# Optimization experiments

Hardware: AMD Instinct MI355X
Metric: run time of the kernel (lower is better)

## Reference

```python
import jax, jax.numpy as jnp
import numpy as np

B, T_ENC, IN, H, SEQ_OUT = 1024, 50, 99, 2112, 25


def _lstm_cell(x, h, c, W_ih, b_ih, W_hh, b_hh):
    # gates: [B, 4H], torch LSTMCell gate order is i, f, g, o
    gates = x @ W_ih.T + b_ih + h @ W_hh.T + b_hh
    i, f, g, o = jnp.split(gates, 4, axis=-1)
    c_new = jax.nn.sigmoid(f) * c + jax.nn.sigmoid(i) * jnp.tanh(g)
    h_new = jax.nn.sigmoid(o) * jnp.tanh(c_new)
    return h_new, c_new


def setup_inputs() -> dict:
    key = jax.random.key(0)
    ks = jax.random.split(key, 14)
    s = 0.04
    return {
        "hidden_states": jax.random.normal(ks[0], (B, T_ENC, H), jnp.float32),
        "cell_states": jax.random.normal(ks[1], (B, T_ENC, H), jnp.float32),
        "global_t_state": jax.random.normal(ks[2], (B, H), jnp.float32),
        "p": jax.random.normal(ks[3], (B, 1, IN), jnp.float32),
        "W_ih0": jax.random.normal(ks[4], (4 * H, IN), jnp.float32) * s,
        "b_ih0": jax.random.normal(ks[5], (4 * H,), jnp.float32) * s,
        "W_hh0": jax.random.normal(ks[6], (4 * H, H), jnp.float32) * s,
        "b_hh0": jax.random.normal(ks[7], (4 * H,), jnp.float32) * s,
        "W_ih1": jax.random.normal(ks[8], (4 * H, H), jnp.float32) * s,
        "b_ih1": jax.random.normal(ks[9], (4 * H,), jnp.float32) * s,
        "W_hh1": jax.random.normal(ks[10], (4 * H, H), jnp.float32) * s,
        "b_hh1": jax.random.normal(ks[11], (4 * H,), jnp.float32) * s,
        "W_out": jax.random.normal(ks[12], (H, IN), jnp.float32) * s,
        "b_out": jax.random.normal(ks[13], (IN,), jnp.float32) * s,
    }


def reference(hidden_states, cell_states, global_t_state, p,
              W_ih0, b_ih0, W_hh0, b_hh0,
              W_ih1, b_ih1, W_hh1, b_hh1,
              W_out, b_out):
    # initial states: layer 0 uses mean over encoder hidden states,
    # layer 1 uses mean over [global_t_state ; hidden_states]
    h0 = hidden_states.mean(axis=1)                                   # [B, H]
    h1 = jnp.concatenate((global_t_state[:, None, :], hidden_states), axis=1).mean(axis=1)
    c0 = cell_states.mean(axis=1)
    c1 = c0
    pre0 = p[:, 0, :]                                                 # seed input [B, IN]

    def step(carry, _):
        h0, c0, h1, c1, prev = carry
        h0n, c0n = _lstm_cell(prev, h0, c0, W_ih0, b_ih0, W_hh0, b_hh0)
        h1n, c1n = _lstm_cell(h0n, h1, c1, W_ih1, b_ih1, W_hh1, b_hh1)
        pre = h1n @ W_out + b_out + prev                              # residual on cell-0 input
        return (h0n, c0n, h1n, c1n, pre), pre

    _, pres = jax.lax.scan(step, (h0, c0, h1, c1, pre0), None, length=SEQ_OUT)
    return pres.transpose(1, 0, 2)                                    # [B, SEQ_OUT, IN]
```

## Files before the change

### kernel.cpp

```cpp
#include <hip/hip_runtime.h>

#define B_    1024
#define H_    2112
#define FH    8448
#define IN_   99
#define TENC  50
#define SEQ   25
#define K0    2240
#define K1    4224
#define LDX0  2240
#define LDX1  4224

typedef __bf16 bf16;
typedef __bf16 bf16x8 __attribute__((ext_vector_type(8)));
typedef __bf16 bf16x4 __attribute__((ext_vector_type(4)));
typedef float  f32x4  __attribute__((ext_vector_type(4)));

__device__ __forceinline__ void gload_lds16(const void* g, void* l) {
  __builtin_amdgcn_global_load_lds(
      (const __attribute__((address_space(1))) void*)g,
      (__attribute__((address_space(3))) void*)l, 16, 0, 0);
}

__device__ __forceinline__ float sigf(float x) { return 1.f / (1.f + __expf(-x)); }
__device__ __forceinline__ float tanhfast(float x) { return 1.f - 2.f / (__expf(2.f * x) + 1.f); }

__global__ __launch_bounds__(128, 3)
void lstm_gemm_cell(const bf16* __restrict__ X, int lda, int K,
                    const bf16* __restrict__ W,
                    const float* __restrict__ bsum,
                    float* __restrict__ Cst,
                    bf16* __restrict__ d1, int ld1,
                    bf16* __restrict__ d2, int ld2)
{
  __shared__ __align__(16) bf16 As[128 * 64];
  __shared__ __align__(16) bf16 Bs[64 * 64];

  const int mb  = blockIdx.x & 7;
  const int hb  = blockIdx.x >> 3;
  const int hc0 = hb * 16;
  const int m0  = mb * 128;

  const int tid  = threadIdx.x;
  const int srow = tid >> 3;
  const int scol = ((tid & 7) ^ (srow & 7)) * 8;

  const bf16* Ab = X + (size_t)(m0 + srow) * lda + scol;
  const bf16* Bb = W + (size_t)(hc0 + srow) * K + scol;

  const int lane = tid & 63;
  const int w    = tid >> 6;
  const int lr   = lane & 15, lq = lane >> 4;
  const int xs   = lr & 7;
  const int cof0 = (lq ^ xs) * 8;
  const int cof1 = ((4 + lq) ^ xs) * 8;

  f32x4 acc[4][4];
#pragma unroll
  for (int a = 0; a < 4; ++a)
#pragma unroll
    for (int b = 0; b < 4; ++b) acc[a][b] = (f32x4){0.f, 0.f, 0.f, 0.f};

  const int KT = K >> 6;
  for (int kt = 0; kt < KT; ++kt) {
    const int ko = kt * 64;
#pragma unroll
    for (int it = 0; it < 8; ++it)
      gload_lds16(Ab + (size_t)it * 16 * lda + ko, &As[it * 1024 + tid * 8]);
#pragma unroll
    for (int it = 0; it < 4; ++it)
      gload_lds16(Bb + (size_t)it * H_ * K + ko, &Bs[it * 1024 + tid * 8]);
    __syncthreads();

    bf16x8 af[4][2], bfr[4][2];
#pragma unroll
    for (int mi = 0; mi < 4; ++mi) {
      const int r = (w * 64 + mi * 16 + lr) * 64;
      af[mi][0] = *(const bf16x8*)&As[r + cof0];
      af[mi][1] = *(const bf16x8*)&As[r + cof1];
    }
#pragma unroll
    for (int nf = 0; nf < 4; ++nf) {
      const int r = (nf * 16 + lr) * 64;
      bfr[nf][0] = *(const bf16x8*)&Bs[r + cof0];
      bfr[nf][1] = *(const bf16x8*)&Bs[r + cof1];
    }
#pragma unroll
    for (int mi = 0; mi < 4; ++mi)
#pragma unroll
      for (int nf = 0; nf < 4; ++nf)
#pragma unroll
        for (int kc = 0; kc < 2; ++kc)
          acc[mi][nf] = __builtin_amdgcn_mfma_f32_16x16x32_bf16(
              af[mi][kc], bfr[nf][kc], acc[mi][nf], 0, 0, 0);
    __syncthreads();
  }

  const int hc = hc0 + lr;
  const float bi  = bsum[hc];
  const float bff = bsum[H_ + hc];
  const float bg  = bsum[2 * H_ + hc];
  const float bo  = bsum[3 * H_ + hc];

#pragma unroll
  for (int mi = 0; mi < 4; ++mi) {
#pragma unroll
    for (int r = 0; r < 4; ++r) {
      const int m = m0 + w * 64 + mi * 16 + lq * 4 + r;
      const float gi = acc[mi][0][r] + bi;
      const float gf = acc[mi][1][r] + bff;
      const float gg = acc[mi][2][r] + bg;
      const float go = acc[mi][3][r] + bo;
      const size_t ci = (size_t)m * H_ + hc;
      const float c_old = Cst[ci];
      const float cn = sigf(gf) * c_old + sigf(gi) * tanhfast(gg);
      const float hn = sigf(go) * tanhfast(cn);
      Cst[ci] = cn;
      const bf16 hb2 = (bf16)hn;
      d1[(size_t)m * ld1 + hc] = hb2;
      if (d2) d2[(size_t)m * ld2 + hc] = hb2;
    }
  }
}

__global__ __launch_bounds__(256, 1)
void out_gemm(const bf16* __restrict__ Hin,
              const bf16* __restrict__ Wo,
              const float* __restrict__ b_out,
              float* __restrict__ prev,
              bf16* __restrict__ X0n,
              float* __restrict__ out, int t)
{
  __shared__ float red[4][4][112];
  const int tid = threadIdx.x;
  const int m0 = blockIdx.x * 4;
  const int lane = tid & 63, wv = tid >> 6;
  const int lr = lane & 15, lq = lane >> 4, lk = lq * 8;

  f32x4 acc[7];
#pragma unroll
  for (int b = 0; b < 7; ++b) acc[b] = (f32x4){0.f, 0.f, 0.f, 0.f};

  const int start = (wv == 0) ? 0 : (1 + wv * 8);
  const int cnt = (wv == 0) ? 9 : 8;

  for (int kt = start; kt < start + cnt; ++kt) {
    const int ko = kt * 64;
    bf16x8 av[2], bv[7][2];
#pragma unroll
    for (int kc = 0; kc < 2; ++kc)
      av[kc] = *(const bf16x8*)&Hin[(size_t)(m0 + (lr & 3)) * LDX1 + ko + kc * 32 + lk];
#pragma unroll
    for (int nf = 0; nf < 7; ++nf)
#pragma unroll
      for (int kc = 0; kc < 2; ++kc)
        bv[nf][kc] = *(const bf16x8*)&Wo[(size_t)(nf * 16 + lr) * H_ + ko + kc * 32 + lk];
#pragma unroll
    for (int nf = 0; nf < 7; ++nf)
#pragma unroll
      for (int kc = 0; kc < 2; ++kc)
        acc[nf] = __builtin_amdgcn_mfma_f32_16x16x32_bf16(av[kc], bv[nf][kc], acc[nf], 0, 0, 0);
  }

  if (lq == 0) {
#pragma unroll
    for (int nf = 0; nf < 7; ++nf)
#pragma unroll
      for (int r = 0; r < 4; ++r)
        red[wv][r][nf * 16 + lr] = acc[nf][r];
  }
  __syncthreads();

  for (int idx = tid; idx < 4 * 112; idx += 256) {
    const int ml = idx / 112, n = idx - ml * 112;
    if (n < IN_) {
      const int m = m0 + ml;
      float s = red[0][ml][n] + red[1][ml][n] + red[2][ml][n] + red[3][ml][n] + b_out[n];
      const float pre = s + prev[m * 112 + n];
      prev[m * 112 + n] = pre;
      out[((size_t)m * SEQ + t) * IN_ + n] = pre;
      X0n[(size_t)m * LDX0 + n] = (bf16)pre;
    }
  }
}

__global__ void init_state(const float* __restrict__ hs, const float* __restrict__ cs,
                           const float* __restrict__ gts,
                           bf16* __restrict__ X0a, bf16* __restrict__ X1a,
                           float* __restrict__ c0, float* __restrict__ c1)
{
  const int h4 = blockIdx.x * 256 + threadIdx.x;
  if (h4 >= 528) return;
  const int b = blockIdx.y;
  const float4* hp = (const float4*)(hs + (size_t)b * TENC * H_) + h4;
  const float4* cp = (const float4*)(cs + (size_t)b * TENC * H_) + h4;
  float4 sh = {0.f, 0.f, 0.f, 0.f}, sc = {0.f, 0.f, 0.f, 0.f};
  for (int tt = 0; tt < TENC; ++tt) {
    float4 a = hp[tt * 528];
    sh.x += a.x; sh.y += a.y; sh.z += a.z; sh.w += a.w;
    float4 c = cp[tt * 528];
    sc.x += c.x; sc.y += c.y; sc.z += c.z; sc.w += c.w;
  }
  const float4 g = ((const float4*)(gts + (size_t)b * H_))[h4];
  const float4 c0v = {sc.x / 50.f, sc.y / 50.f, sc.z / 50.f, sc.w / 50.f};
  ((float4*)(c0 + (size_t)b * H_))[h4] = c0v;
  ((float4*)(c1 + (size_t)b * H_))[h4] = c0v;
  bf16x4 h0b = {(bf16)(sh.x / 50.f), (bf16)(sh.y / 50.f), (bf16)(sh.z / 50.f), (bf16)(sh.w / 50.f)};
  *(bf16x4*)&X0a[(size_t)b * LDX0 + 128 + h4 * 4] = h0b;
  bf16x4 h1b = {(bf16)((sh.x + g.x) / 51.f), (bf16)((sh.y + g.y) / 51.f),
                (bf16)((sh.z + g.z) / 51.f), (bf16)((sh.w + g.w) / 51.f)};
  *(bf16x4*)&X1a[(size_t)b * LDX1 + 2112 + h4 * 4] = h1b;
}

__global__ void init_prev(const float* __restrict__ p, float* __restrict__ prev,
                          bf16* __restrict__ X0a, bf16* __restrict__ X0b)
{
  const int idx = blockIdx.x * 256 + threadIdx.x;
  const int b = idx >> 7, n = idx & 127;
  const float v = (n < IN_) ? p[(size_t)b * IN_ + n] : 0.f;
  if (n < 112) prev[b * 112 + n] = v;
  X0a[(size_t)b * LDX0 + n] = (bf16)v;
  X0b[(size_t)b * LDX0 + n] = (bf16)0.f;
}

__global__ void pack_w0(const float* __restrict__ Wih, const float* __restrict__ Whh,
                        bf16* __restrict__ Wc)
{
  const int n = blockIdx.x;
  const float* a = Wih + (size_t)n * IN_;
  const float* b = Whh + (size_t)n * H_;
  bf16* d = Wc + (size_t)n * K0;
  for (int k = threadIdx.x; k < K0; k += 256) {
    float v = (k < IN_) ? a[k] : ((k >= 128) ? b[k - 128] : 0.f);
    d[k] = (bf16)v;
  }
}

__global__ void pack_w1(const float* __restrict__ Wih, const float* __restrict__ Whh,
                        bf16* __restrict__ Wc)
{
  const int n = blockIdx.x;
  bf16* d = Wc + (size_t)n * K1;
  for (int k = threadIdx.x; k < K1; k += 256)
    d[k] = (bf16)((k < H_) ? Wih[(size_t)n * H_ + k] : Whh[(size_t)n * H_ + k - H_]);
}

__global__ void pack_wo(const float* __restrict__ W, bf16* __restrict__ Wo)
{
  const int n = blockIdx.x;
  for (int k = threadIdx.x; k < H_; k += 256)
    Wo[(size_t)n * H_ + k] = (n < IN_) ? (bf16)W[(size_t)k * IN_ + n] : (bf16)0.f;
}

__global__ void pack_bias(const float* __restrict__ bi0, const float* __restrict__ bh0,
                          const float* __restrict__ bi1, const float* __restrict__ bh1,
                          float* __restrict__ bs0, float* __restrict__ bs1)
{
  const int i = blockIdx.x * 256 + threadIdx.x;
  if (i < FH) { bs0[i] = bi0[i] + bh0[i]; bs1[i] = bi1[i] + bh1[i]; }
}

extern "C" void kernel_launch(void* const* d_in, const int* in_sizes, int n_in,
                              void* d_out, int out_size, void* d_ws, size_t ws_size,
                              hipStream_t stream)
{
  (void)in_sizes; (void)n_in; (void)out_size; (void)ws_size;
  const float* hs   = (const float*)d_in[0];
  const float* cs   = (const float*)d_in[1];
  const float* gts  = (const float*)d_in[2];
  const float* p    = (const float*)d_in[3];
  const float* Wih0 = (const float*)d_in[4];
  const float* bih0 = (const float*)d_in[5];
  const float* Whh0 = (const float*)d_in[6];
  const float* bhh0 = (const float*)d_in[7];
  const float* Wih1 = (const float*)d_in[8];
  const float* bih1 = (const float*)d_in[9];
  const float* Whh1 = (const float*)d_in[10];
  const float* bhh1 = (const float*)d_in[11];
  const float* Wout = (const float*)d_in[12];
  const float* bout = (const float*)d_in[13];
  float* out = (float*)d_out;

  char* ws = (char*)d_ws;
  size_t off = 0;
  auto alloc = [&](size_t bytes) -> void* {
    void* q = ws + off; off += (bytes + 255) & ~(size_t)255; return q;
  };
  bf16* Wc0 = (bf16*)alloc((size_t)FH * K0 * 2);
  bf16* Wc1 = (bf16*)alloc((size_t)FH * K1 * 2);
  bf16* Wo  = (bf16*)alloc((size_t)112 * H_ * 2);
  float* bs0 = (float*)alloc((size_t)FH * 4);
  float* bs1 = (float*)alloc((size_t)FH * 4);
  bf16* X0[2] = {(bf16*)alloc((size_t)B_ * LDX0 * 2), (bf16*)alloc((size_t)B_ * LDX0 * 2)};
  bf16* X1[2] = {(bf16*)alloc((size_t)B_ * LDX1 * 2), (bf16*)alloc((size_t)B_ * LDX1 * 2)};
  float* c0  = (float*)alloc((size_t)B_ * H_ * 4);
  float* c1  = (float*)alloc((size_t)B_ * H_ * 4);
  float* prev = (float*)alloc((size_t)B_ * 112 * 4);

  pack_w0<<<FH, 256, 0, stream>>>(Wih0, Whh0, Wc0);
  pack_w1<<<FH, 256, 0, stream>>>(Wih1, Whh1, Wc1);
  pack_wo<<<112, 256, 0, stream>>>(Wout, Wo);
  pack_bias<<<(FH + 255) / 256, 256, 0, stream>>>(bih0, bhh0, bih1, bhh1, bs0, bs1);
  init_prev<<<(B_ * 128) / 256, 256, 0, stream>>>(p, prev, X0[0], X0[1]);
  init_state<<<dim3(3, B_), 256, 0, stream>>>(hs, cs, gts, X0[0], X1[0], c0, c1);

  for (int t = 0; t < SEQ; ++t) {
    const int cur = t & 1, nxt = cur ^ 1;
    lstm_gemm_cell<<<1056, 128, 0, stream>>>(
        X0[cur], LDX0, K0, Wc0, bs0, c0, X1[cur], LDX1, X0[nxt] + 128, LDX0);
    lstm_gemm_cell<<<1056, 128, 0, stream>>>(
        X1[cur], LDX1, K1, Wc1, bs1, c1, X1[nxt] + 2112, LDX1, (bf16*)nullptr, 0);
    out_gemm<<<256, 256, 0, stream>>>(X1[nxt] + 2112, Wo, bout, prev, X0[nxt], out, t);
  }
}
```

Baseline: 5.315 ms.

## Pre-pack LSTM weights in MFMA fragment order and load directly to registers

Weights are repacked once into per-tile MFMA fragment order so each lane loads its B fragments straight from global memory into registers, dropping the Bs LDS buffer and its staging loads. Block indices are also remapped so consecutive blocks share the same weight tile across the 8 M-blocks rather than the same A rows, aiming for better L2 reuse of weights. The trade-off is that global-to-register weight loads now sit on each k-step's critical path with no LDS double-buffering, and the per-k-step LDS footprint shrinks.

```diff
diff --git a/kernel.cpp b/kernel.cpp
--- a/kernel.cpp
+++ b/kernel.cpp
@@ -10,6 +10,9 @@
 #define K1    4224
 #define LDX0  2240
 #define LDX1  4224
+#define KT0   35
+#define KT1   66
+#define HB_   132
 
 typedef __bf16 bf16;
 typedef __bf16 bf16x8 __attribute__((ext_vector_type(8)));
@@ -27,26 +30,24 @@
 
 __global__ __launch_bounds__(128, 3)
 void lstm_gemm_cell(const bf16* __restrict__ X, int lda, int K,
-                    const bf16* __restrict__ W,
+                    const bf16* __restrict__ Wpk,
                     const float* __restrict__ bsum,
                     float* __restrict__ Cst,
                     bf16* __restrict__ d1, int ld1,
                     bf16* __restrict__ d2, int ld2)
 {
   __shared__ __align__(16) bf16 As[128 * 64];
-  __shared__ __align__(16) bf16 Bs[64 * 64];
-
-  const int mb  = blockIdx.x & 7;
-  const int hb  = blockIdx.x >> 3;
+
+  const int vid = (blockIdx.x & 7) * 132 + (blockIdx.x >> 3);
+  const int hb  = vid >> 3;
   const int hc0 = hb * 16;
-  const int m0  = mb * 128;
+  const int m0  = (vid & 7) * 128;
 
   const int tid  = threadIdx.x;
   const int srow = tid >> 3;
   const int scol = ((tid & 7) ^ (srow & 7)) * 8;
 
   const bf16* Ab = X + (size_t)(m0 + srow) * lda + scol;
-  const bf16* Bb = W + (size_t)(hc0 + srow) * K + scol;
 
   const int lane = tid & 63;
   const int w    = tid >> 6;
@@ -55,35 +56,36 @@
   const int cof0 = (lq ^ xs) * 8;
   const int cof1 = ((4 + lq) ^ xs) * 8;
 
+  const int KT = K >> 6;
+  const bf16* Wp = Wpk + (size_t)hb * KT * 4096 + lane * 8;
+
   f32x4 acc[4][4];
 #pragma unroll
   for (int a = 0; a < 4; ++a)
 #pragma unroll
     for (int b = 0; b < 4; ++b) acc[a][b] = (f32x4){0.f, 0.f, 0.f, 0.f};
 
-  const int KT = K >> 6;
   for (int kt = 0; kt < KT; ++kt) {
     const int ko = kt * 64;
 #pragma unroll
     for (int it = 0; it < 8; ++it)
       gload_lds16(Ab + (size_t)it * 16 * lda + ko, &As[it * 1024 + tid * 8]);
-#pragma unroll
-    for (int it = 0; it < 4; ++it)
-      gload_lds16(Bb + (size_t)it * H_ * K + ko, &Bs[it * 1024 + tid * 8]);
+
+    const bf16* Wt = Wp + (size_t)kt * 4096;
+    bf16x8 bfr[4][2];
+#pragma unroll
+    for (int nf = 0; nf < 4; ++nf) {
+      bfr[nf][0] = *(const bf16x8*)&Wt[(nf * 2 + 0) * 512];
+      bfr[nf][1] = *(const bf16x8*)&Wt[(nf * 2 + 1) * 512];
+    }
     __syncthreads();
 
-    bf16x8 af[4][2], bfr[4][2];
+    bf16x8 af[4][2];
 #pragma unroll
     for (int mi = 0; mi < 4; ++mi) {
       const int r = (w * 64 + mi * 16 + lr) * 64;
       af[mi][0] = *(const bf16x8*)&As[r + cof0];
       af[mi][1] = *(const bf16x8*)&As[r + cof1];
-    }
-#pragma unroll
-    for (int nf = 0; nf < 4; ++nf) {
-      const int r = (nf * 16 + lr) * 64;
-      bfr[nf][0] = *(const bf16x8*)&Bs[r + cof0];
-      bfr[nf][1] = *(const bf16x8*)&Bs[r + cof1];
     }
 #pragma unroll
     for (int mi = 0; mi < 4; ++mi)
@@ -223,26 +225,54 @@
   X0b[(size_t)b * LDX0 + n] = (bf16)0.f;
 }
 
-__global__ void pack_w0(const float* __restrict__ Wih, const float* __restrict__ Whh,
-                        bf16* __restrict__ Wc)
-{
-  const int n = blockIdx.x;
-  const float* a = Wih + (size_t)n * IN_;
-  const float* b = Whh + (size_t)n * H_;
-  bf16* d = Wc + (size_t)n * K0;
-  for (int k = threadIdx.x; k < K0; k += 256) {
-    float v = (k < IN_) ? a[k] : ((k >= 128) ? b[k - 128] : 0.f);
-    d[k] = (bf16)v;
-  }
-}
-
-__global__ void pack_w1(const float* __restrict__ Wih, const float* __restrict__ Whh,
-                        bf16* __restrict__ Wc)
-{
-  const int n = blockIdx.x;
-  bf16* d = Wc + (size_t)n * K1;
-  for (int k = threadIdx.x; k < K1; k += 256)
-    d[k] = (bf16)((k < H_) ? Wih[(size_t)n * H_ + k] : Whh[(size_t)n * H_ + k - H_]);
+__global__ void pack_w0_frag(const float* __restrict__ Wih, const float* __restrict__ Whh,
+                             bf16* __restrict__ Wpk)
+{
+  const int kt = blockIdx.x, hb = blockIdx.y;
+  const int lane = threadIdx.x;
+  const int lr = lane & 15, lq = lane >> 4;
+  bf16* dst = Wpk + (((size_t)hb * KT0 + kt) * 8) * 512 + lane * 8;
+#pragma unroll
+  for (int fi = 0; fi < 8; ++fi) {
+    const int nf = fi >> 1, kc = fi & 1;
+    const int row = nf * H_ + hb * 16 + lr;
+    const int k0 = kt * 64 + kc * 32 + lq * 8;
+    bf16x8 v;
+#pragma unroll
+    for (int e = 0; e < 8; ++e) {
+      const int k = k0 + e;
+      float f;
+      if (k < IN_)        f = Wih[(size_t)row * IN_ + k];
+      else if (k < 128)   f = 0.f;
+      else                f = Whh[(size_t)row * H_ + (k - 128)];
+      v[e] = (bf16)f;
+    }
+    *(bf16x8*)(dst + fi * 512) = v;
+  }
+}
+
+__global__ void pack_w1_frag(const float* __restrict__ Wih, const float* __restrict__ Whh,
+                             bf16* __restrict__ Wpk)
+{
+  const int kt = blockIdx.x, hb = blockIdx.y;
+  const int lane = threadIdx.x;
+  const int lr = lane & 15, lq = lane >> 4;
+  bf16* dst = Wpk + (((size_t)hb * KT1 + kt) * 8) * 512 + lane * 8;
+#pragma unroll
+  for (int fi = 0; fi < 8; ++fi) {
+    const int nf = fi >> 1, kc = fi & 1;
+    const int row = nf * H_ + hb * 16 + lr;
+    const int k0 = kt * 64 + kc * 32 + lq * 8;
+    bf16x8 v;
+#pragma unroll
+    for (int e = 0; e < 8; ++e) {
+      const int k = k0 + e;
+      const float f = (k < H_) ? Wih[(size_t)row * H_ + k]
+                               : Whh[(size_t)row * H_ + (k - H_)];
+      v[e] = (bf16)f;
+    }
+    *(bf16x8*)(dst + fi * 512) = v;
+  }
 }
 
 __global__ void pack_wo(const float* __restrict__ W, bf16* __restrict__ Wo)
@@ -286,8 +316,8 @@
   auto alloc = [&](size_t bytes) -> void* {
     void* q = ws + off; off += (bytes + 255) & ~(size_t)255; return q;
   };
-  bf16* Wc0 = (bf16*)alloc((size_t)FH * K0 * 2);
-  bf16* Wc1 = (bf16*)alloc((size_t)FH * K1 * 2);
+  bf16* Wc0 = (bf16*)alloc((size_t)HB_ * KT0 * 4096 * 2);
+  bf16* Wc1 = (bf16*)alloc((size_t)HB_ * KT1 * 4096 * 2);
   bf16* Wo  = (bf16*)alloc((size_t)112 * H_ * 2);
   float* bs0 = (float*)alloc((size_t)FH * 4);
   float* bs1 = (float*)alloc((size_t)FH * 4);
@@ -297,8 +327,8 @@
   float* c1  = (float*)alloc((size_t)B_ * H_ * 4);
   float* prev = (float*)alloc((size_t)B_ * 112 * 4);
 
-  pack_w0<<<FH, 256, 0, stream>>>(Wih0, Whh0, Wc0);
-  pack_w1<<<FH, 256, 0, stream>>>(Wih1, Whh1, Wc1);
+  pack_w0_frag<<<dim3(KT0, HB_), 64, 0, stream>>>(Wih0, Whh0, Wc0);
+  pack_w1_frag<<<dim3(KT1, HB_), 64, 0, stream>>>(Wih1, Whh1, Wc1);
   pack_wo<<<112, 256, 0, stream>>>(Wout, Wo);
   pack_bias<<<(FH + 255) / 256, 256, 0, stream>>>(bih0, bhh0, bih1, bhh1, bs0, bs1);
   init_prev<<<(B_ * 128) / 256, 256, 0, stream>>>(p, prev, X0[0], X0[1]);
```

After: 5.012 ms. 1.06x faster.

## Double-buffer LSTM gate GEMM with larger tiles and remapped block order

Applied to the files above, without the earlier changes.

Rewrites the fused LSTM gate GEMM to use 256-thread blocks computing 128x128 tiles (32 hidden units × 4 gates) with K-step 32 and double-buffered LDS, so the next tile's async loads overlap the current MFMAs. It also remaps the block index so consecutive blocks share weight slices across the batch tiles. The XOR swizzle is dropped, which may introduce LDS bank conflicts, and fewer, larger blocks reduce the number of waves available to hide latency.

```diff
diff --git a/kernel.cpp b/kernel.cpp
--- a/kernel.cpp
+++ b/kernel.cpp
@@ -25,7 +25,7 @@
 __device__ __forceinline__ float sigf(float x) { return 1.f / (1.f + __expf(-x)); }
 __device__ __forceinline__ float tanhfast(float x) { return 1.f - 2.f / (__expf(2.f * x) + 1.f); }
 
-__global__ __launch_bounds__(128, 3)
+__global__ __launch_bounds__(256, 2)
 void lstm_gemm_cell(const bf16* __restrict__ X, int lda, int K,
                     const bf16* __restrict__ W,
                     const float* __restrict__ bsum,
@@ -33,27 +33,28 @@
                     bf16* __restrict__ d1, int ld1,
                     bf16* __restrict__ d2, int ld2)
 {
-  __shared__ __align__(16) bf16 As[128 * 64];
-  __shared__ __align__(16) bf16 Bs[64 * 64];
-
-  const int mb  = blockIdx.x & 7;
-  const int hb  = blockIdx.x >> 3;
-  const int hc0 = hb * 16;
-  const int m0  = mb * 128;
+  __shared__ __align__(16) bf16 As0[128 * 32];
+  __shared__ __align__(16) bf16 As1[128 * 32];
+  __shared__ __align__(16) bf16 Bs0[128 * 32];
+  __shared__ __align__(16) bf16 Bs1[128 * 32];
+
+  const int vid = (blockIdx.x & 7) * 66 + (blockIdx.x >> 3);
+  const int hb  = vid >> 3;
+  const int hc0 = hb * 32;
+  const int m0  = (vid & 7) * 128;
 
   const int tid  = threadIdx.x;
-  const int srow = tid >> 3;
-  const int scol = ((tid & 7) ^ (srow & 7)) * 8;
+  const int srow = tid >> 2;
+  const int scol = (tid & 3) * 8;
 
   const bf16* Ab = X + (size_t)(m0 + srow) * lda + scol;
-  const bf16* Bb = W + (size_t)(hc0 + srow) * K + scol;
+  const bf16* Bb = W + ((size_t)((srow >> 5) * H_ + hc0 + (srow & 31))) * K + scol;
+  const size_t HK2 = (size_t)2 * H_ * K;
 
   const int lane = tid & 63;
-  const int w    = tid >> 6;
-  const int lr   = lane & 15, lq = lane >> 4;
-  const int xs   = lr & 7;
-  const int cof0 = (lq ^ xs) * 8;
-  const int cof1 = ((4 + lq) ^ xs) * 8;
+  const int wv = tid >> 6;
+  const int wm = wv >> 1, wn = wv & 1;
+  const int lr = lane & 15, lq = lane >> 4;
 
   f32x4 acc[4][4];
 #pragma unroll
@@ -61,42 +62,45 @@
 #pragma unroll
     for (int b = 0; b < 4; ++b) acc[a][b] = (f32x4){0.f, 0.f, 0.f, 0.f};
 
-  const int KT = K >> 6;
-  for (int kt = 0; kt < KT; ++kt) {
-    const int ko = kt * 64;
-#pragma unroll
-    for (int it = 0; it < 8; ++it)
-      gload_lds16(Ab + (size_t)it * 16 * lda + ko, &As[it * 1024 + tid * 8]);
-#pragma unroll
-    for (int it = 0; it < 4; ++it)
-      gload_lds16(Bb + (size_t)it * H_ * K + ko, &Bs[it * 1024 + tid * 8]);
+#define STAGE(kt, AD, BD) do {                                              \
+    const int ko_ = (kt) * 32;                                              \
+    gload_lds16(Ab + (size_t)0 * lda + ko_,  &AD[0 * 2048 + tid * 8]);      \
+    gload_lds16(Ab + (size_t)64 * lda + ko_, &AD[1 * 2048 + tid * 8]);      \
+    gload_lds16(Bb + ko_,                    &BD[0 * 2048 + tid * 8]);      \
+    gload_lds16(Bb + HK2 + ko_,              &BD[1 * 2048 + tid * 8]);      \
+  } while (0)
+
+#define COMPUTE(AS, BS) do {                                                \
+    bf16x8 af_[4], bf_[4];                                                  \
+    _Pragma("unroll")                                                       \
+    for (int mi = 0; mi < 4; ++mi)                                          \
+      af_[mi] = *(const bf16x8*)&AS[(wm * 64 + mi * 16 + lr) * 32 + lq * 8];\
+    _Pragma("unroll")                                                       \
+    for (int nf = 0; nf < 4; ++nf)                                          \
+      bf_[nf] = *(const bf16x8*)&BS[(nf * 32 + wn * 16 + lr) * 32 + lq * 8];\
+    _Pragma("unroll")                                                       \
+    for (int mi = 0; mi < 4; ++mi)                                          \
+      _Pragma("unroll")                                                     \
+      for (int nf = 0; nf < 4; ++nf)                                        \
+        acc[mi][nf] = __builtin_amdgcn_mfma_f32_16x16x32_bf16(              \
+            af_[mi], bf_[nf], acc[mi][nf], 0, 0, 0);                        \
+  } while (0)
+
+  const int KT = K >> 5;
+  STAGE(0, As0, Bs0);
+  __syncthreads();
+  for (int kt = 0; kt < KT; kt += 2) {
+    STAGE(kt + 1, As1, Bs1);
+    COMPUTE(As0, Bs0);
     __syncthreads();
-
-    bf16x8 af[4][2], bfr[4][2];
-#pragma unroll
-    for (int mi = 0; mi < 4; ++mi) {
-      const int r = (w * 64 + mi * 16 + lr) * 64;
-      af[mi][0] = *(const bf16x8*)&As[r + cof0];
-      af[mi][1] = *(const bf16x8*)&As[r + cof1];
-    }
-#pragma unroll
-    for (int nf = 0; nf < 4; ++nf) {
-      const int r = (nf * 16 + lr) * 64;
-      bfr[nf][0] = *(const bf16x8*)&Bs[r + cof0];
-      bfr[nf][1] = *(const bf16x8*)&Bs[r + cof1];
-    }
-#pragma unroll
-    for (int mi = 0; mi < 4; ++mi)
-#pragma unroll
-      for (int nf = 0; nf < 4; ++nf)
-#pragma unroll
-        for (int kc = 0; kc < 2; ++kc)
-          acc[mi][nf] = __builtin_amdgcn_mfma_f32_16x16x32_bf16(
-              af[mi][kc], bfr[nf][kc], acc[mi][nf], 0, 0, 0);
+    if (kt + 2 < KT) STAGE(kt + 2, As0, Bs0);
+    COMPUTE(As1, Bs1);
     __syncthreads();
   }
-
-  const int hc = hc0 + lr;
+#undef STAGE
+#undef COMPUTE
+
+  const int hc = hc0 + wn * 16 + lr;
   const float bi  = bsum[hc];
   const float bff = bsum[H_ + hc];
   const float bg  = bsum[2 * H_ + hc];
@@ -106,7 +110,7 @@
   for (int mi = 0; mi < 4; ++mi) {
 #pragma unroll
     for (int r = 0; r < 4; ++r) {
-      const int m = m0 + w * 64 + mi * 16 + lq * 4 + r;
+      const int m = m0 + wm * 64 + mi * 16 + lq * 4 + r;
       const float gi = acc[mi][0][r] + bi;
       const float gf = acc[mi][1][r] + bff;
       const float gg = acc[mi][2][r] + bg;
@@ -306,9 +310,9 @@
 
   for (int t = 0; t < SEQ; ++t) {
     const int cur = t & 1, nxt = cur ^ 1;
-    lstm_gemm_cell<<<1056, 128, 0, stream>>>(
+    lstm_gemm_cell<<<528, 256, 0, stream>>>(
         X0[cur], LDX0, K0, Wc0, bs0, c0, X1[cur], LDX1, X0[nxt] + 128, LDX0);
-    lstm_gemm_cell<<<1056, 128, 0, stream>>>(
+    lstm_gemm_cell<<<528, 256, 0, stream>>>(
         X1[cur], LDX1, K1, Wc1, bs1, c1, X1[nxt] + 2112, LDX1, (bf16*)nullptr, 0);
     out_gemm<<<256, 256, 0, stream>>>(X1[nxt] + 2112, Wo, bout, prev, X0[nxt], out, t);
   }
```

New measurement: 4.666 ms. -12.2%, faster.
